# Kernel optimization log

Measured on AMD Instinct MI355X. Metric: run time of the kernel, lower is better.

Reference implementation:

```python
import jax, jax.numpy as jnp
import numpy as np

SIZE = 1024
LATENT_DIM = 256
BETA_C = 0.25
LEGACY = True


def setup_inputs() -> dict:
    key = jax.random.key(0)
    k1, k2 = jax.random.split(key)
    z = jax.random.normal(k1, (8, LATENT_DIM, 16, 16, 16), dtype=jnp.float32)
    # nn.Embedding weight initialized uniform(-1/size, 1/size)
    embedding = jax.random.uniform(
        k2, (SIZE, LATENT_DIM), minval=-1.0 / SIZE, maxval=1.0 / SIZE, dtype=jnp.float32
    )
    return {"z": z, "embedding": embedding}


def reference(z, embedding):
    sg = jax.lax.stop_gradient
    B, C, D, H, W = z.shape
    # [B, D, H, W, C]
    zp = jnp.transpose(z, (0, 2, 3, 4, 1))
    zf = zp.reshape(-1, C)  # [N, C]
    # pairwise squared distances [N, K]
    d = (
        jnp.sum(zf * zf, axis=1, keepdims=True)
        + jnp.sum(embedding * embedding, axis=1)
        - 2.0 * (zf @ embedding.T)
    )
    idx = jnp.argmin(d, axis=1)  # [N]
    # direct gather == one-hot @ embedding
    z_q = embedding[idx].reshape(zp.shape)
    if LEGACY:
        loss = jnp.mean((sg(z_q) - zp) ** 2) + BETA_C * jnp.mean((z_q - sg(zp)) ** 2)
    else:
        loss = BETA_C * jnp.mean((sg(z_q) - zp) ** 2) + jnp.mean((z_q - sg(zp)) ** 2)
    # perplexity: e_mean = mean of one-hot encodings == normalized counts
    counts = jnp.zeros((SIZE,), dtype=z.dtype).at[idx].add(1.0)
    e_mean = counts / zf.shape[0]
    perplexity = jnp.exp(-jnp.sum(e_mean * jnp.log(e_mean + 1e-10)))
    # straight-through estimator
    z_q = zp + sg(z_q - zp)
    z_q = jnp.transpose(z_q, (0, 4, 1, 2, 3))  # back to [B, C, D, H, W]
    return z_q, loss, perplexity, idx
```

## Files before the change

### kernel.cpp

```cpp
#include <hip/hip_runtime.h>
#include <cstddef>
#include <cstdint>

#define CDIM 256
#define SPAT 4096
#define KCODE 1024

#define LOSS_OFF 8388608
#define PERP_OFF 8388609
#define IDX_OFF  8388610

typedef __bf16 bf16x8 __attribute__((ext_vector_type(8)));
typedef float floatx16 __attribute__((ext_vector_type(16)));
typedef unsigned short ushort8 __attribute__((ext_vector_type(8)));

__device__ __forceinline__ unsigned short f2bf_rne(float f) {
    union { float f; uint32_t u; } c; c.f = f;
    uint32_t u = c.u;
    return (unsigned short)((u + 0x7fffu + ((u >> 16) & 1u)) >> 16);
}
__device__ __forceinline__ float bf2f(unsigned short h) {
    union { float f; uint32_t u; } c; c.u = ((uint32_t)h) << 16;
    return c.f;
}

__device__ __forceinline__ void dma16(const void* g, void* l) {
    __builtin_amdgcn_global_load_lds(
        (const __attribute__((address_space(1))) void*)g,
        (__attribute__((address_space(3))) void*)l, 16, 0, 0);
}

__global__ __launch_bounds__(256) void vq_prep(const float* __restrict__ emb,
                                               unsigned short* __restrict__ ehsw,
                                               unsigned short* __restrict__ elsw,
                                               float* __restrict__ enorm,
                                               float* __restrict__ counts,
                                               float* __restrict__ losssum) {
    int tid = threadIdx.x;
    if (blockIdx.x == 0) {
        for (int i = tid; i < KCODE; i += 256) counts[i] = 0.0f;
        if (tid == 0) losssum[0] = 0.0f;
    }
    int w = tid >> 6, lane = tid & 63;
    int k = blockIdx.x * 4 + w;
    const float* row = emb + (size_t)k * CDIM;
    float s = 0.0f;
#pragma unroll
    for (int i = 0; i < 4; ++i) {
        float v = row[lane + 64 * i];
        s = fmaf(v, v, s);
    }
#pragma unroll
    for (int m = 32; m > 0; m >>= 1) s += __shfl_xor(s, m, 64);
    if (lane == 0) enorm[k] = s;

    float4 v4 = *(const float4*)(row + lane * 4);
    unsigned short h0 = f2bf_rne(v4.x), h1 = f2bf_rne(v4.y),
                   h2 = f2bf_rne(v4.z), h3 = f2bf_rne(v4.w);
    ushort4 hv = make_ushort4(h0, h1, h2, h3);
    ushort4 lv = make_ushort4(f2bf_rne(v4.x - bf2f(h0)), f2bf_rne(v4.y - bf2f(h1)),
                              f2bf_rne(v4.z - bf2f(h2)), f2bf_rne(v4.w - bf2f(h3)));
    int kb = lane >> 1, cj = (lane & 1) * 4;
    int st = k >> 5, ks = k & 31;
    int phys = kb ^ (ks & 7);
    size_t dst = (size_t)st * 8192 + ks * 256 + phys * 8 + cj;
    *(ushort4*)(ehsw + dst) = hv;
    *(ushort4*)(elsw + dst) = lv;
}

__global__ __launch_bounds__(512, 2) void vq_main(const float* __restrict__ z,
                                                  const float* __restrict__ emb,
                                                  const unsigned short* __restrict__ ehsw,
                                                  const unsigned short* __restrict__ elsw,
                                                  const float* __restrict__ enorm,
                                                  float* __restrict__ counts,
                                                  float* __restrict__ losssum,
                                                  float* __restrict__ out) {
    __shared__ __align__(16) unsigned char lds[131072 + 4096 + 512 + 1024 + 1024 + 512];
    float* zhalf = (float*)lds;
    float* ens_s = (float*)(lds + 131072);
    float* zzs   = (float*)(lds + 135168);
    float* pb_s  = (float*)(lds + 135680);
    int*   pb_i  = (int*)(lds + 136704);
    int*   bidxs = (int*)(lds + 137728);

    const int tid = threadIdx.x;
    const int w = tid >> 6;
    const int lane = tid & 63;
    const int m_ = lane & 31;
    const int g = lane >> 5;
    const int kh = w >> 2;
    const int cq = w & 3;
    const int ch = cq & 1;
    const int hlf = cq >> 1;
    const int n0 = blockIdx.x * 128;
    const int b = n0 >> 12;
    const int sp0 = n0 & 4095;
    const float* zb = z + (size_t)b * CDIM * SPAT + sp0;

    const int stg0 = (blockIdx.x >> 3) & 15;

    ushort8 zh[16], zl[16];

    for (int h = 0; h < 2; ++h) {
        for (int i = tid; i < CDIM * 16; i += 512) {
            int c = i >> 4, seg = i & 15;
            *(float4*)&zhalf[c * 64 + seg * 4] =
                *(const float4*)(zb + (size_t)c * SPAT + h * 64 + seg * 4);
        }
        __syncthreads();
        if (hlf == h) {
#pragma unroll
            for (int kc = 0; kc < 16; ++kc) {
#pragma unroll
                for (int j = 0; j < 8; ++j) {
                    float v = zhalf[(kc * 16 + g * 8 + j) * 64 + ch * 32 + m_];
                    unsigned short hb = f2bf_rne(v);
                    unsigned short lb = f2bf_rne(v - bf2f(hb));
                    zh[kc][j] = hb; zl[kc][j] = lb;
                }
            }
        } else if (w == (h == 0 ? 2 : 0)) {
            float s = 0.0f;
            for (int c = 0; c < CDIM; ++c) {
                float v = zhalf[c * 64 + lane];
                s = fmaf(v, v, s);
            }
            zzs[h * 64 + lane] = s;
        } else if (h == 0 && w == 3) {
            for (int i = lane; i < KCODE; i += 64) ens_s[i] = enorm[i];
        }
        __syncthreads();
    }

    const float zzv = zzs[cq * 32 + m_];

    float bs = 3.4e38f;
    int bi_ = 0;

    const int bufid = w >> 1;
    const int hf = w & 1;
    const char* gsrc = (const char*)((bufid & 1) ? elsw : ehsw);
    const int gs0 = kh * 16;

    {
        const char* gp = gsrc + ((size_t)(gs0 + stg0) << 14) + (hf << 13) + (lane << 4);
        char* lp = (char*)lds + ((size_t)bufid << 14) + (hf << 13);
#pragma unroll
        for (int j = 0; j < 8; ++j) dma16(gp + j * 1024, lp + j * 1024);
    }

    for (int s = 0; s < 16; ++s) {
        __syncthreads();
        if (s < 15) {
            const int se_n = (s + 1 + stg0) & 15;
            const char* gp = gsrc + ((size_t)(gs0 + se_n) << 14) + (hf << 13) + (lane << 4);
            char* lp = (char*)lds + (((size_t)(s + 1) & 1) << 16) +
                       ((size_t)bufid << 14) + (hf << 13);
#pragma unroll
            for (int j = 0; j < 8; ++j) dma16(gp + j * 1024, lp + j * 1024);
            __builtin_amdgcn_sched_barrier(0);
        }
        const char* EHb = (const char*)lds + (((size_t)s & 1) << 16) + ((size_t)kh << 15);
        const char* ELb = EHb + 16384;

        floatx16 a = {0.0f, 0.0f, 0.0f, 0.0f, 0.0f, 0.0f, 0.0f, 0.0f,
                      0.0f, 0.0f, 0.0f, 0.0f, 0.0f, 0.0f, 0.0f, 0.0f};
#pragma unroll
        for (int kc = 0; kc < 16; ++kc) {
            int kb0 = kc * 2 + g;
            int off = m_ * 512 + ((kb0 ^ (m_ & 7)) << 4);
            bf16x8 aeh = *(const bf16x8*)(EHb + off);
            bf16x8 ael = *(const bf16x8*)(ELb + off);
            bf16x8 bh = __builtin_bit_cast(bf16x8, zh[kc]);
            bf16x8 bl = __builtin_bit_cast(bf16x8, zl[kc]);
            a = __builtin_amdgcn_mfma_f32_32x32x16_bf16(aeh, bh, a, 0, 0, 0);
            a = __builtin_amdgcn_mfma_f32_32x32x16_bf16(ael, bh, a, 0, 0, 0);
            a = __builtin_amdgcn_mfma_f32_32x32x16_bf16(aeh, bl, a, 0, 0, 0);
        }

        const int se = (s + stg0) & 15;
#pragma unroll
        for (int reg = 0; reg < 16; ++reg) {
            int mm = (reg & 3) + 8 * (reg >> 2) + 4 * g;
            int code = kh * 512 + se * 32 + mm;
            float en = ens_s[code];
            float d = (zzv + en) - 2.0f * a[reg];
            if (d < bs || (d == bs && code < bi_)) { bs = d; bi_ = code; }
        }
    }

    {
        float s2 = __shfl_xor(bs, 32, 64);
        int i2 = __shfl_xor(bi_, 32, 64);
        if (s2 < bs || (s2 == bs && i2 < bi_)) { bs = s2; bi_ = i2; }
    }
    __syncthreads();
    if (lane < 32) {
        pb_s[kh * 128 + cq * 32 + m_] = bs;
        pb_i[kh * 128 + cq * 32 + m_] = bi_;
    }
    __syncthreads();
    if (tid < 128) {
        float s0 = pb_s[tid], s1 = pb_s[128 + tid];
        int i0 = pb_i[tid], i1 = pb_i[128 + tid];
        int ki = (s1 < s0) ? i1 : i0;
        bidxs[tid] = ki;
        out[IDX_OFF + n0 + tid] = (float)ki;
        atomicAdd(&counts[ki], 1.0f);
    }
    __syncthreads();

#pragma unroll
    for (int r = 0; r < 16; ++r) {
        int row = w * 16 + r;
        int k = bidxs[row];
        int slot = (row & 3) * 32 + (row >> 2);
        dma16((const char*)emb + ((size_t)k << 10) + (lane << 4),
              (char*)lds + (size_t)slot * 1040);
    }
    __syncthreads();

    if (tid < 256) {
        float ls = 0.0f;
        float* outz = out + (size_t)b * CDIM * SPAT + sp0;
        const int col4 = tid & 31;
        const int c_0 = tid >> 5;
        const float* e0 = (const float*)((const char*)lds + (size_t)(0 * 32 + col4) * 1040);
        const float* e1 = (const float*)((const char*)lds + (size_t)(1 * 32 + col4) * 1040);
        const float* e2 = (const float*)((const char*)lds + (size_t)(2 * 32 + col4) * 1040);
        const float* e3 = (const float*)((const char*)lds + (size_t)(3 * 32 + col4) * 1040);
        for (int c = c_0; c < CDIM; c += 8) {
            float4 zp = *(const float4*)(zb + (size_t)c * SPAT + col4 * 4);
            float d0 = e0[c] - zp.x, d1 = e1[c] - zp.y,
                  d2 = e2[c] - zp.z, d3 = e3[c] - zp.w;
            float4 o;
            o.x = zp.x + d0; o.y = zp.y + d1; o.z = zp.z + d2; o.w = zp.w + d3;
            ls = fmaf(d0, d0, ls); ls = fmaf(d1, d1, ls);
            ls = fmaf(d2, d2, ls); ls = fmaf(d3, d3, ls);
            *(float4*)(outz + (size_t)c * SPAT + col4 * 4) = o;
        }
#pragma unroll
        for (int m = 32; m > 0; m >>= 1) ls += __shfl_xor(ls, m, 64);
        if (lane == 0) atomicAdd(losssum, ls);
    }
}

__global__ __launch_bounds__(256) void vq_finalize(const float* __restrict__ counts,
                                                   const float* __restrict__ losssum,
                                                   float* __restrict__ out) {
    __shared__ float red[256];
    int tid = threadIdx.x;
    float s = 0.0f;
    for (int k = tid; k < KCODE; k += 256) {
        float em = counts[k] * (1.0f / 32768.0f);
        s += em * logf(em + 1e-10f);
    }
    red[tid] = s;
    __syncthreads();
    for (int off = 128; off > 0; off >>= 1) {
        if (tid < off) red[tid] += red[tid + off];
        __syncthreads();
    }
    if (tid == 0) {
        float m = losssum[0] * (1.0f / 8388608.0f);
        out[LOSS_OFF] = m + 0.25f * m;
        out[PERP_OFF] = expf(-red[0]);
    }
}

extern "C" void kernel_launch(void* const* d_in, const int* in_sizes, int n_in,
                              void* d_out, int out_size, void* d_ws, size_t ws_size,
                              hipStream_t stream) {
    const float* z = (const float*)d_in[0];
    const float* emb = (const float*)d_in[1];
    float* out = (float*)d_out;
    unsigned short* ehsw = (unsigned short*)d_ws;
    unsigned short* elsw = ehsw + (size_t)KCODE * CDIM;
    float* enorm = (float*)(elsw + (size_t)KCODE * CDIM);
    float* counts = enorm + KCODE;
    float* losssum = counts + KCODE;

    vq_prep<<<256, 256, 0, stream>>>(emb, ehsw, elsw, enorm, counts, losssum);
    vq_main<<<256, 512, 0, stream>>>(z, emb, ehsw, elsw, enorm, counts, losssum, out);
    vq_finalize<<<1, 256, 0, stream>>>(counts, losssum, out);
}
```

Measured before the change: 171.6 us.

## Split VQ main kernel into distance and gather kernels with atomicMin argmin

The fused main kernel is split into a distance kernel with 512 blocks of 256 threads, each handling one half of the codebook for 128 positions, and a separate gather/loss kernel. The two codebook halves are combined through a 64-bit atomicMin on a packed (distance bits, index) key. This doubles the block count and halves LDS per block, aiming for better occupancy and CU coverage. The cost is an extra kernel launch, re-reading z in the distance kernel across two blocks, and global atomics. Packing the float bits as an unsigned key only orders correctly for non-negative distances, so a slightly negative rounded distance could pick the wrong code.

```diff
diff --git a/kernel.cpp b/kernel.cpp
--- a/kernel.cpp
+++ b/kernel.cpp
@@ -35,12 +35,15 @@
                                                unsigned short* __restrict__ elsw,
                                                float* __restrict__ enorm,
                                                float* __restrict__ counts,
-                                               float* __restrict__ losssum) {
+                                               float* __restrict__ losssum,
+                                               unsigned long long* __restrict__ pbm) {
     int tid = threadIdx.x;
     if (blockIdx.x == 0) {
         for (int i = tid; i < KCODE; i += 256) counts[i] = 0.0f;
         if (tid == 0) losssum[0] = 0.0f;
     }
+    if (tid < 128) pbm[blockIdx.x * 128 + tid] = 0xFFFFFFFFFFFFFFFFull;
+
     int w = tid >> 6, lane = tid & 63;
     int k = blockIdx.x * 4 + w;
     const float* row = emb + (size_t)k * CDIM;
@@ -68,42 +71,36 @@
     *(ushort4*)(elsw + dst) = lv;
 }
 
-__global__ __launch_bounds__(512, 2) void vq_main(const float* __restrict__ z,
-                                                  const float* __restrict__ emb,
+__global__ __launch_bounds__(256, 2) void vq_dist(const float* __restrict__ z,
                                                   const unsigned short* __restrict__ ehsw,
                                                   const unsigned short* __restrict__ elsw,
                                                   const float* __restrict__ enorm,
-                                                  float* __restrict__ counts,
-                                                  float* __restrict__ losssum,
-                                                  float* __restrict__ out) {
-    __shared__ __align__(16) unsigned char lds[131072 + 4096 + 512 + 1024 + 1024 + 512];
+                                                  unsigned long long* __restrict__ pbm) {
+    __shared__ __align__(16) unsigned char lds[65536 + 2048 + 512];
     float* zhalf = (float*)lds;
-    float* ens_s = (float*)(lds + 131072);
-    float* zzs   = (float*)(lds + 135168);
-    float* pb_s  = (float*)(lds + 135680);
-    int*   pb_i  = (int*)(lds + 136704);
-    int*   bidxs = (int*)(lds + 137728);
+    float* ens_s = (float*)(lds + 65536);
+    float* zzs   = (float*)(lds + 67584);
 
     const int tid = threadIdx.x;
     const int w = tid >> 6;
     const int lane = tid & 63;
     const int m_ = lane & 31;
     const int g = lane >> 5;
-    const int kh = w >> 2;
-    const int cq = w & 3;
-    const int ch = cq & 1;
-    const int hlf = cq >> 1;
-    const int n0 = blockIdx.x * 128;
+    const int bid = blockIdx.x;
+    const int pos = bid >> 1;
+    const int kh = bid & 1;
+    const int ch = w & 1;
+    const int hlf = w >> 1;
+    const int n0 = pos * 128;
     const int b = n0 >> 12;
     const int sp0 = n0 & 4095;
     const float* zb = z + (size_t)b * CDIM * SPAT + sp0;
-
-    const int stg0 = (blockIdx.x >> 3) & 15;
+    const int stg0 = (bid >> 4) & 15;
 
     ushort8 zh[16], zl[16];
 
     for (int h = 0; h < 2; ++h) {
-        for (int i = tid; i < CDIM * 16; i += 512) {
+        for (int i = tid; i < CDIM * 16; i += 256) {
             int c = i >> 4, seg = i & 15;
             *(float4*)&zhalf[c * 64 + seg * 4] =
                 *(const float4*)(zb + (size_t)c * SPAT + h * 64 + seg * 4);
@@ -128,19 +125,19 @@
             }
             zzs[h * 64 + lane] = s;
         } else if (h == 0 && w == 3) {
-            for (int i = lane; i < KCODE; i += 64) ens_s[i] = enorm[i];
+            for (int i = lane; i < 512; i += 64) ens_s[i] = enorm[kh * 512 + i];
         }
         __syncthreads();
     }
 
-    const float zzv = zzs[cq * 32 + m_];
+    const float zzv = zzs[w * 32 + m_];
 
     float bs = 3.4e38f;
     int bi_ = 0;
 
     const int bufid = w >> 1;
     const int hf = w & 1;
-    const char* gsrc = (const char*)((bufid & 1) ? elsw : ehsw);
+    const char* gsrc = (const char*)(bufid ? elsw : ehsw);
     const int gs0 = kh * 16;
 
     {
@@ -155,13 +152,13 @@
         if (s < 15) {
             const int se_n = (s + 1 + stg0) & 15;
             const char* gp = gsrc + ((size_t)(gs0 + se_n) << 14) + (hf << 13) + (lane << 4);
-            char* lp = (char*)lds + (((size_t)(s + 1) & 1) << 16) +
+            char* lp = (char*)lds + (((size_t)(s + 1) & 1) << 15) +
                        ((size_t)bufid << 14) + (hf << 13);
 #pragma unroll
             for (int j = 0; j < 8; ++j) dma16(gp + j * 1024, lp + j * 1024);
             __builtin_amdgcn_sched_barrier(0);
         }
-        const char* EHb = (const char*)lds + (((size_t)s & 1) << 16) + ((size_t)kh << 15);
+        const char* EHb = (const char*)lds + (((size_t)s & 1) << 15);
         const char* ELb = EHb + 16384;
 
         floatx16 a = {0.0f, 0.0f, 0.0f, 0.0f, 0.0f, 0.0f, 0.0f, 0.0f,
@@ -183,9 +180,10 @@
 #pragma unroll
         for (int reg = 0; reg < 16; ++reg) {
             int mm = (reg & 3) + 8 * (reg >> 2) + 4 * g;
-            int code = kh * 512 + se * 32 + mm;
-            float en = ens_s[code];
+            int il = se * 32 + mm;
+            float en = ens_s[il];
             float d = (zzv + en) - 2.0f * a[reg];
+            int code = kh * 512 + il;
             if (d < bs || (d == bs && code < bi_)) { bs = d; bi_ = code; }
         }
     }
@@ -195,16 +193,32 @@
         int i2 = __shfl_xor(bi_, 32, 64);
         if (s2 < bs || (s2 == bs && i2 < bi_)) { bs = s2; bi_ = i2; }
     }
-    __syncthreads();
     if (lane < 32) {
-        pb_s[kh * 128 + cq * 32 + m_] = bs;
-        pb_i[kh * 128 + cq * 32 + m_] = bi_;
-    }
-    __syncthreads();
+        unsigned long long key =
+            ((unsigned long long)__float_as_uint(bs) << 32) | (unsigned int)bi_;
+        atomicMin(&pbm[n0 + w * 32 + m_], key);
+    }
+}
+
+__global__ __launch_bounds__(256) void vq_gather(const float* __restrict__ z,
+                                                 const float* __restrict__ emb,
+                                                 const unsigned long long* __restrict__ pbm,
+                                                 float* __restrict__ counts,
+                                                 float* __restrict__ losssum,
+                                                 float* __restrict__ out) {
+    __shared__ __align__(16) unsigned char lds[128 * 1040 + 512];
+    int* bidxs = (int*)(lds + 133120);
+
+    const int tid = threadIdx.x;
+    const int w = tid >> 6;
+    const int lane = tid & 63;
+    const int n0 = blockIdx.x * 128;
+    const int b = n0 >> 12;
+    const int sp0 = n0 & 4095;
+    const float* zb = z + (size_t)b * CDIM * SPAT + sp0;
+
     if (tid < 128) {
-        float s0 = pb_s[tid], s1 = pb_s[128 + tid];
-        int i0 = pb_i[tid], i1 = pb_i[128 + tid];
-        int ki = (s1 < s0) ? i1 : i0;
+        int ki = (int)(unsigned int)(pbm[n0 + tid] & 0xFFFFFFFFull);
         bidxs[tid] = ki;
         out[IDX_OFF + n0 + tid] = (float)ki;
         atomicAdd(&counts[ki], 1.0f);
@@ -212,8 +226,8 @@
     __syncthreads();
 
 #pragma unroll
-    for (int r = 0; r < 16; ++r) {
-        int row = w * 16 + r;
+    for (int r = 0; r < 32; ++r) {
+        int row = w * 32 + r;
         int k = bidxs[row];
         int slot = (row & 3) * 32 + (row >> 2);
         dma16((const char*)emb + ((size_t)k << 10) + (lane << 4),
@@ -221,29 +235,27 @@
     }
     __syncthreads();
 
-    if (tid < 256) {
-        float ls = 0.0f;
-        float* outz = out + (size_t)b * CDIM * SPAT + sp0;
-        const int col4 = tid & 31;
-        const int c_0 = tid >> 5;
-        const float* e0 = (const float*)((const char*)lds + (size_t)(0 * 32 + col4) * 1040);
-        const float* e1 = (const float*)((const char*)lds + (size_t)(1 * 32 + col4) * 1040);
-        const float* e2 = (const float*)((const char*)lds + (size_t)(2 * 32 + col4) * 1040);
-        const float* e3 = (const float*)((const char*)lds + (size_t)(3 * 32 + col4) * 1040);
-        for (int c = c_0; c < CDIM; c += 8) {
-            float4 zp = *(const float4*)(zb + (size_t)c * SPAT + col4 * 4);
-            float d0 = e0[c] - zp.x, d1 = e1[c] - zp.y,
-                  d2 = e2[c] - zp.z, d3 = e3[c] - zp.w;
-            float4 o;
-            o.x = zp.x + d0; o.y = zp.y + d1; o.z = zp.z + d2; o.w = zp.w + d3;
-            ls = fmaf(d0, d0, ls); ls = fmaf(d1, d1, ls);
-            ls = fmaf(d2, d2, ls); ls = fmaf(d3, d3, ls);
-            *(float4*)(outz + (size_t)c * SPAT + col4 * 4) = o;
-        }
-#pragma unroll
-        for (int m = 32; m > 0; m >>= 1) ls += __shfl_xor(ls, m, 64);
-        if (lane == 0) atomicAdd(losssum, ls);
-    }
+    float ls = 0.0f;
+    float* outz = out + (size_t)b * CDIM * SPAT + sp0;
+    const int col4 = tid & 31;
+    const int c_0 = tid >> 5;
+    const float* e0 = (const float*)((const char*)lds + (size_t)(0 * 32 + col4) * 1040);
+    const float* e1 = (const float*)((const char*)lds + (size_t)(1 * 32 + col4) * 1040);
+    const float* e2 = (const float*)((const char*)lds + (size_t)(2 * 32 + col4) * 1040);
+    const float* e3 = (const float*)((const char*)lds + (size_t)(3 * 32 + col4) * 1040);
+    for (int c = c_0; c < CDIM; c += 8) {
+        float4 zp = *(const float4*)(zb + (size_t)c * SPAT + col4 * 4);
+        float d0 = e0[c] - zp.x, d1 = e1[c] - zp.y,
+              d2 = e2[c] - zp.z, d3 = e3[c] - zp.w;
+        float4 o;
+        o.x = zp.x + d0; o.y = zp.y + d1; o.z = zp.z + d2; o.w = zp.w + d3;
+        ls = fmaf(d0, d0, ls); ls = fmaf(d1, d1, ls);
+        ls = fmaf(d2, d2, ls); ls = fmaf(d3, d3, ls);
+        *(float4*)(outz + (size_t)c * SPAT + col4 * 4) = o;
+    }
+#pragma unroll
+    for (int m = 32; m > 0; m >>= 1) ls += __shfl_xor(ls, m, 64);
+    if (lane == 0) atomicAdd(losssum, ls);
 }
 
 __global__ __launch_bounds__(256) void vq_finalize(const float* __restrict__ counts,
@@ -275,13 +287,15 @@
     const float* z = (const float*)d_in[0];
     const float* emb = (const float*)d_in[1];
     float* out = (float*)d_out;
-    unsigned short* ehsw = (unsigned short*)d_ws;
+    unsigned long long* pbm = (unsigned long long*)d_ws;
+    unsigned short* ehsw = (unsigned short*)(pbm + 32768);
     unsigned short* elsw = ehsw + (size_t)KCODE * CDIM;
     float* enorm = (float*)(elsw + (size_t)KCODE * CDIM);
     float* counts = enorm + KCODE;
     float* losssum = counts + KCODE;
 
-    vq_prep<<<256, 256, 0, stream>>>(emb, ehsw, elsw, enorm, counts, losssum);
-    vq_main<<<256, 512, 0, stream>>>(z, emb, ehsw, elsw, enorm, counts, losssum, out);
+    vq_prep<<<256, 256, 0, stream>>>(emb, ehsw, elsw, enorm, counts, losssum, pbm);
+    vq_dist<<<512, 256, 0, stream>>>(z, ehsw, elsw, enorm, pbm);
+    vq_gather<<<256, 256, 0, stream>>>(z, emb, pbm, counts, losssum, out);
     vq_finalize<<<1, 256, 0, stream>>>(counts, losssum, out);
 }
```

Result: slower. 179.8 us (+4.8%).
